# Kernel optimization log

Hardware: AMD Instinct MI355X
Metric: run time of the kernel (lower is better)

## Reference

```python
import jax, jax.numpy as jnp
import numpy as np

N = 100_000
E = 3_200_000
NCLASS = 64
TOPK = 16
NHID = 128
DEGREE = 6


def setup_inputs() -> dict:
    key = jax.random.key(0)
    ks = jax.random.split(key, 8)
    x = jax.random.normal(ks[0], (N, NCLASS), dtype=jnp.float32)
    edge_row = jax.random.randint(ks[1], (E,), 0, N, dtype=jnp.int64)
    edge_col = jax.random.randint(ks[2], (E,), 0, N, dtype=jnp.int64)
    edge_val = jax.random.uniform(ks[3], (E,), dtype=jnp.float32) / 32.0  # ~row-normalized
    # torch.nn.Linear init: U(-1/sqrt(fan_in), 1/sqrt(fan_in))
    lim1 = 1.0 / np.sqrt(TOPK)
    lim2 = 1.0 / np.sqrt(NHID)
    W1 = jax.random.uniform(ks[4], (NHID, TOPK), jnp.float32, -lim1, lim1)
    b1 = jnp.zeros((NHID,), jnp.float32)
    W2 = jax.random.uniform(ks[5], (DEGREE, NHID), jnp.float32, -lim2, lim2)
    b2 = jnp.zeros((DEGREE,), jnp.float32)
    return {"x": x, "edge_row": edge_row, "edge_col": edge_col,
            "edge_val": edge_val, "W1": W1, "b1": b1, "W2": W2, "b2": b2}


def _spmm(edge_row, edge_col, edge_val, h):
    # (adj @ h)[i] = sum_{(i,j) in E} val_ij * h[j]
    return jax.ops.segment_sum(edge_val[:, None] * h[edge_col], edge_row,
                               num_segments=N)


def reference(x, edge_row, edge_col, edge_val, W1, b1, W2, b2):
    # gating: softmax over classes -> top-k probs -> small MLP -> hop weights
    p = jax.nn.softmax(x, axis=1)
    tk, _ = jax.lax.top_k(p, TOPK)                       # [N, TOPK]
    h = jax.nn.leaky_relu(tk @ W1.T + b1, 0.1)           # [N, NHID]
    weight = jax.nn.softmax(h @ W2.T + b2, axis=1)       # [N, DEGREE]
    # dropout is identity in eval mode
    out = weight[:, 0:1] * x
    cur = x
    for i in range(DEGREE - 1):
        cur = _spmm(edge_row, edge_col, edge_val, cur)
        out = out + weight[:, i + 1:i + 2] * cur
    return jax.nn.log_softmax(out, axis=1)
```

## Files before the change

### kernel.cpp

```cpp
#include <hip/hip_runtime.h>
#include <math.h>

#define N_NODES 100000
#define N_EDGES 3200000
#define NCLASS  64
#define TOPK    16
#define NHID    128
#define DEG     6

#define NBUCK   391
#define NSEG    8
#define SEGCAP  1408

#define EB ((N_EDGES + 255) / 256)
#define GNODES 32
#define GB ((N_NODES + GNODES - 1) / GNODES)

__device__ __forceinline__ float bf2f(unsigned short u) {
    return __uint_as_float(((unsigned)u) << 16);
}
__device__ __forceinline__ unsigned short f2bf(float f) {
    unsigned u = __float_as_uint(f);
    u = (u + 0x7FFFu + ((u >> 16) & 1u)) >> 16;
    return (unsigned short)u;
}

__device__ __forceinline__ float wave_max(float v) {
    #pragma unroll
    for (int off = 1; off < 64; off <<= 1) v = fmaxf(v, __shfl_xor(v, off));
    return v;
}
__device__ __forceinline__ float wave_sum(float v) {
    #pragma unroll
    for (int off = 1; off < 64; off <<= 1) v += __shfl_xor(v, off);
    return v;
}

__global__ __launch_bounds__(256) void scatter_gating_kernel(
        const int* __restrict__ erow, const int* __restrict__ ecol,
        const float* __restrict__ eval, int* __restrict__ fill,
        int2* __restrict__ staging,
        const float* __restrict__ x,  const float* __restrict__ W1,
        const float* __restrict__ b1, const float* __restrict__ W2,
        const float* __restrict__ b2, float* __restrict__ weight,
        float* __restrict__ out_acc, unsigned short* __restrict__ xbf) {
    __shared__ float sW1t[TOPK * NHID];
    __shared__ float sb1[NHID];
    __shared__ float sW2[DEG * NHID];
    __shared__ float sb2[DEG];

    if (blockIdx.x < EB) {
        int i = blockIdx.x * 256 + threadIdx.x;
        int s = blockIdx.x & 7;
        if (i < N_EDGES) {
            int   r = __builtin_nontemporal_load(&erow[i]);
            int   c = __builtin_nontemporal_load(&ecol[i]);
            float w = __builtin_nontemporal_load(&eval[i]);
            int b = r >> 8;
            int pos = atomicAdd(&fill[(s * NBUCK + b) * 16], 1);
            if (pos < SEGCAP) {
                int2 e;
                e.x = (c << 8) | (r & 255);
                e.y = __float_as_int(w);
                staging[((size_t)b * NSEG + s) * SEGCAP + pos] = e;
            }
        }
        return;
    }

    int tid = threadIdx.x;
    for (int idx = tid; idx < NHID * TOPK; idx += 256) {
        int k = idx / NHID, j = idx - k * NHID;
        sW1t[idx] = W1[j * TOPK + k];
    }
    for (int i = tid; i < NHID; i += 256) sb1[i] = b1[i];
    for (int i = tid; i < DEG * NHID; i += 256) sW2[i] = W2[i];
    if (tid < DEG) sb2[tid] = b2[tid];
    __syncthreads();

    int wave = tid >> 6;
    int lane = tid & 63;
    int gb = blockIdx.x - EB;

    for (int it = 0; it < GNODES / 4; it++) {
        int node = gb * GNODES + it * 4 + wave;
        if (node >= N_NODES) continue;

        float xv = x[node * NCLASS + lane];
        xbf[node * NCLASS + lane] = f2bf(xv);

        float v = xv;
        #pragma unroll
        for (int k = 2; k <= 64; k <<= 1) {
            #pragma unroll
            for (int j = k >> 1; j > 0; j >>= 1) {
                float o = __shfl_xor(v, j);
                bool keep_small = (((lane & j) == 0) == ((lane & k) == 0));
                v = keep_small ? fminf(v, o) : fmaxf(v, o);
            }
        }
        float m = __shfl(v, 63);
        float e = __expf(v - m);
        float s = wave_sum(e);
        float inv_s = 1.0f / s;

        float h0 = sb1[lane], h1 = sb1[lane + 64];
        #pragma unroll
        for (int k = 0; k < TOPK; k++) {
            float sv = __shfl(v, 63 - k);
            float tk = __expf(sv - m) * inv_s;
            h0 += tk * sW1t[k * NHID + lane];
            h1 += tk * sW1t[k * NHID + lane + 64];
        }
        h0 = (h0 > 0.f) ? h0 : 0.1f * h0;
        h1 = (h1 > 0.f) ? h1 : 0.1f * h1;

        float w[DEG];
        float wm = -1e30f;
        #pragma unroll
        for (int d = 0; d < DEG; d++) {
            float part = h0 * sW2[d * NHID + lane] + h1 * sW2[d * NHID + lane + 64];
            w[d] = wave_sum(part) + sb2[d];
            wm = fmaxf(wm, w[d]);
        }
        float wsum = 0.f;
        #pragma unroll
        for (int d = 0; d < DEG; d++) { w[d] = __expf(w[d] - wm); wsum += w[d]; }
        float inv = 1.0f / wsum;

        if (lane < DEG) weight[node * DEG + lane] = w[lane] * inv;
        out_acc[node * NCLASS + lane] = w[0] * inv * xv;
    }
}

__global__ __launch_bounds__(256) void phase2_build(
        const int2* __restrict__ staging, const int* __restrict__ fill,
        int* __restrict__ row_ptr, int2* __restrict__ edges_s) {
    __shared__ int lred[256];
    __shared__ int lhist[256];
    __shared__ int lscan[256];
    __shared__ int lfill[256];
    __shared__ int sseg[NSEG];
    int b = blockIdx.x, tid = threadIdx.x;

    int part = 0;
    for (int j = tid; j < b; j += 256) {
        int t = 0;
        #pragma unroll
        for (int s = 0; s < NSEG; s++) t += min(fill[(s * NBUCK + j) * 16], SEGCAP);
        part += t;
    }
    lred[tid] = part;
    if (tid < NSEG) sseg[tid] = min(fill[(tid * NBUCK + b) * 16], SEGCAP);
    __syncthreads();
    for (int off = 128; off > 0; off >>= 1) {
        if (tid < off) lred[tid] += lred[tid + off];
        __syncthreads();
    }
    int base_b = lred[0];

    lhist[tid] = 0;
    __syncthreads();
    for (int s = 0; s < NSEG; s++) {
        int c = sseg[s];
        const int2* seg = staging + ((size_t)b * NSEG + s) * SEGCAP;
        for (int j = tid; j < c; j += 256) atomicAdd(&lhist[seg[j].x & 255], 1);
    }
    __syncthreads();
    int v = lhist[tid];
    lscan[tid] = v;
    __syncthreads();
    for (int off = 1; off < 256; off <<= 1) {
        int t = (tid >= off) ? lscan[tid - off] : 0;
        __syncthreads();
        lscan[tid] += t;
        __syncthreads();
    }
    int excl = base_b + (lscan[tid] - v);
    int grow = b * 256 + tid;
    if (grow < N_NODES) row_ptr[grow] = excl;
    if (b == NBUCK - 1 && tid == 255) row_ptr[N_NODES] = excl + v;
    lfill[tid] = excl;
    __syncthreads();
    for (int s = 0; s < NSEG; s++) {
        int c = sseg[s];
        const int2* seg = staging + ((size_t)b * NSEG + s) * SEGCAP;
        for (int j = tid; j < c; j += 256) {
            int2 e = seg[j];
            int rl = e.x & 255;
            int pos = atomicAdd(&lfill[rl], 1);
            edges_s[pos] = make_int2((int)(((unsigned)e.x) >> 8), e.y);
        }
    }
}

__device__ __forceinline__ void gather8(const unsigned short* __restrict__ src,
                                        const long long* __restrict__ edq,
                                        int e, int lane, float& acc) {
    long long q[8];
    #pragma unroll
    for (int k = 0; k < 8; k++) q[k] = __builtin_nontemporal_load(&edq[e + k]);
    float vk[8], fk[8];
    #pragma unroll
    for (int k = 0; k < 8; k++) {
        int col = __builtin_amdgcn_readfirstlane((int)(unsigned)q[k]);
        vk[k] = __int_as_float(__builtin_amdgcn_readfirstlane((int)(q[k] >> 32)));
        fk[k] = bf2f(src[col * NCLASS + lane]);
    }
    #pragma unroll
    for (int k = 0; k < 8; k++) acc += vk[k] * fk[k];
}

__device__ __forceinline__ void gather4(const unsigned short* __restrict__ src,
                                        const long long* __restrict__ edq,
                                        int e, int lane, float& acc) {
    long long q[4];
    #pragma unroll
    for (int k = 0; k < 4; k++) q[k] = __builtin_nontemporal_load(&edq[e + k]);
    float vk[4], fk[4];
    #pragma unroll
    for (int k = 0; k < 4; k++) {
        int col = __builtin_amdgcn_readfirstlane((int)(unsigned)q[k]);
        vk[k] = __int_as_float(__builtin_amdgcn_readfirstlane((int)(q[k] >> 32)));
        fk[k] = bf2f(src[col * NCLASS + lane]);
    }
    #pragma unroll
    for (int k = 0; k < 4; k++) acc += vk[k] * fk[k];
}

__device__ __forceinline__ float drain_row(const unsigned short* __restrict__ src,
                                           const long long* __restrict__ edq,
                                           int e, int end, int lane, float acc) {
    for (; e + 4 <= end; e += 4) gather4(src, edq, e, lane, acc);
    for (; e < end; e++) {
        long long q0 = __builtin_nontemporal_load(&edq[e]);
        int   c0 = __builtin_amdgcn_readfirstlane((int)(unsigned)q0);
        float v0 = __int_as_float(__builtin_amdgcn_readfirstlane((int)(q0 >> 32)));
        acc += v0 * bf2f(src[c0 * NCLASS + lane]);
    }
    return acc;
}

__global__ __launch_bounds__(256) void spmm_kernel(
        const unsigned short* __restrict__ src, unsigned short* __restrict__ dst,
        const unsigned short* __restrict__ prev2,
        const int* __restrict__ row_ptr, const int2* __restrict__ edges_s,
        const float* __restrict__ weight,
        float* __restrict__ out_acc, float* __restrict__ final_out,
        int hop, int mode) {
    int wave = threadIdx.x >> 6;
    int lane = threadIdx.x & 63;
    int wid = blockIdx.x * 4 + wave;
    int rA = wid * 2;
    if (rA >= N_NODES) return;
    int rB = rA + 1;

    int sA   = __builtin_amdgcn_readfirstlane(row_ptr[rA]);
    int endA = __builtin_amdgcn_readfirstlane(row_ptr[rA + 1]);
    int endB = __builtin_amdgcn_readfirstlane(row_ptr[rA + 2]);

    const long long* edq = (const long long*)edges_s;
    float accA = 0.f, accB = 0.f;
    int eA = sA, eB = endA;
    while (eA + 8 <= endA && eB + 8 <= endB) {
        gather8(src, edq, eA, lane, accA);
        gather8(src, edq, eB, lane, accB);
        eA += 8; eB += 8;
    }
    accA = drain_row(src, edq, eA, endA, lane, accA);
    accB = drain_row(src, edq, eB, endB, lane, accB);

    float wA = weight[rA * DEG + hop];
    float wB = weight[rB * DEG + hop];
    if (mode == 0) {
        dst[rA * NCLASS + lane] = f2bf(accA);
        dst[rB * NCLASS + lane] = f2bf(accB);
    } else if (mode == 1) {
        dst[rA * NCLASS + lane] = f2bf(accA);
        dst[rB * NCLASS + lane] = f2bf(accB);
        float pA = bf2f(src[rA * NCLASS + lane]);
        float pB = bf2f(src[rB * NCLASS + lane]);
        float wpA = weight[rA * DEG + hop - 1];
        float wpB = weight[rB * DEG + hop - 1];
        out_acc[rA * NCLASS + lane] += wpA * pA + wA * accA;
        out_acc[rB * NCLASS + lane] += wpB * pB + wB * accB;
    } else {
        float p1A = bf2f(src[rA * NCLASS + lane]);
        float p1B = bf2f(src[rB * NCLASS + lane]);
        float p2A = bf2f(prev2[rA * NCLASS + lane]);
        float p2B = bf2f(prev2[rB * NCLASS + lane]);
        float vA = out_acc[rA * NCLASS + lane]
                 + weight[rA * DEG + hop - 2] * p2A
                 + weight[rA * DEG + hop - 1] * p1A + wA * accA;
        float mA = wave_max(vA);
        float eA2 = __expf(vA - mA);
        float sA2 = wave_sum(eA2);
        final_out[rA * NCLASS + lane] = vA - mA - __logf(sA2);

        float vB = out_acc[rB * NCLASS + lane]
                 + weight[rB * DEG + hop - 2] * p2B
                 + weight[rB * DEG + hop - 1] * p1B + wB * accB;
        float mB = wave_max(vB);
        float eB2 = __expf(vB - mB);
        float sB2 = wave_sum(eB2);
        final_out[rB * NCLASS + lane] = vB - mB - __logf(sB2);
    }
}

extern "C" void kernel_launch(void* const* d_in, const int* in_sizes, int n_in,
                              void* d_out, int out_size, void* d_ws, size_t ws_size,
                              hipStream_t stream) {
    const float* x    = (const float*)d_in[0];
    const int*   erow = (const int*)  d_in[1];
    const int*   ecol = (const int*)  d_in[2];
    const float* eval = (const float*)d_in[3];
    const float* W1   = (const float*)d_in[4];
    const float* b1   = (const float*)d_in[5];
    const float* W2   = (const float*)d_in[6];
    const float* b2   = (const float*)d_in[7];
    float* out = (float*)d_out;

    char* ws = (char*)d_ws;
    size_t off = 0;
    auto alloc = [&](size_t bytes) -> void* {
        void* p = ws + off;
        off = (off + bytes + 255) & ~(size_t)255;
        return p;
    };
    char* regionS = (char*)alloc((size_t)NBUCK * NSEG * SEGCAP * 8);
    int2* staging = (int2*)regionS;
    unsigned short* cur0 = (unsigned short*)regionS;
    unsigned short* cur1 = (unsigned short*)(regionS + (size_t)N_NODES * NCLASS * 2);
    unsigned short* xbf  = (unsigned short*)alloc((size_t)N_NODES * NCLASS * 2);

    int2*  edges_s = (int2*)alloc((size_t)N_EDGES * 8);
    int*   row_ptr = (int*) alloc((size_t)(N_NODES + 1) * 4);
    int*   fill    = (int*) alloc((size_t)NSEG * NBUCK * 16 * 4);
    float* weight  = (float*)alloc((size_t)N_NODES * DEG * 4);

    const int WB = ((N_NODES / 2) + 3) / 4;

    hipMemsetAsync(fill, 0, (size_t)NSEG * NBUCK * 16 * 4, stream);
    scatter_gating_kernel<<<EB + GB, 256, 0, stream>>>(
        erow, ecol, eval, fill, staging, x, W1, b1, W2, b2, weight, out, xbf);
    phase2_build<<<NBUCK, 256, 0, stream>>>(staging, fill, row_ptr, edges_s);

    spmm_kernel<<<WB, 256, 0, stream>>>(xbf,  cur0, cur0, row_ptr, edges_s, weight, out, out, 1, 0);
    spmm_kernel<<<WB, 256, 0, stream>>>(cur0, cur1, cur0, row_ptr, edges_s, weight, out, out, 2, 1);
    spmm_kernel<<<WB, 256, 0, stream>>>(cur1, cur0, cur0, row_ptr, edges_s, weight, out, out, 3, 0);
    spmm_kernel<<<WB, 256, 0, stream>>>(cur0, cur1, cur0, row_ptr, edges_s, weight, out, out, 4, 0);
    spmm_kernel<<<WB, 256, 0, stream>>>(cur1, cur0, cur0, row_ptr, edges_s, weight, out, out, 5, 3);
}
```

Baseline: 682.4 us.

## Interleave gating blocks among scatter blocks and process four rows per wave in SpMM

The fused scatter/gating kernel now interleaves block roles so every fifth block runs gating and the rest scatter edges. Gating work is spread across the grid instead of all running at the tail. The SpMM kernel now has each wave handle four consecutive rows with four independent gather streams instead of two, which exposes more memory-level parallelism per wave. The cost is more registers and half as many waves, which could reduce occupancy or load balance.

Measured after the change: 670.9 us. Within noise of the previous version (-1.7%).

```diff
diff --git a/kernel.cpp b/kernel.cpp
--- a/kernel.cpp
+++ b/kernel.cpp
@@ -49,9 +49,11 @@
     __shared__ float sW2[DEG * NHID];
     __shared__ float sb2[DEG];
 
-    if (blockIdx.x < EB) {
-        int i = blockIdx.x * 256 + threadIdx.x;
-        int s = blockIdx.x & 7;
+    unsigned bi = blockIdx.x;
+    if (bi % 5 != 0) {
+        int sid = (int)(bi - bi / 5u - 1u);
+        int i = sid * 256 + threadIdx.x;
+        int s = sid & 7;
         if (i < N_EDGES) {
             int   r = __builtin_nontemporal_load(&erow[i]);
             int   c = __builtin_nontemporal_load(&ecol[i]);
@@ -68,6 +70,7 @@
         return;
     }
 
+    int gb = (int)(bi / 5u);
     int tid = threadIdx.x;
     for (int idx = tid; idx < NHID * TOPK; idx += 256) {
         int k = idx / NHID, j = idx - k * NHID;
@@ -80,7 +83,6 @@
 
     int wave = tid >> 6;
     int lane = tid & 63;
-    int gb = blockIdx.x - EB;
 
     for (int it = 0; it < GNODES / 4; it++) {
         int node = gb * GNODES + it * 4 + wave;
@@ -251,59 +253,53 @@
     int wave = threadIdx.x >> 6;
     int lane = threadIdx.x & 63;
     int wid = blockIdx.x * 4 + wave;
-    int rA = wid * 2;
-    if (rA >= N_NODES) return;
-    int rB = rA + 1;
-
-    int sA   = __builtin_amdgcn_readfirstlane(row_ptr[rA]);
-    int endA = __builtin_amdgcn_readfirstlane(row_ptr[rA + 1]);
-    int endB = __builtin_amdgcn_readfirstlane(row_ptr[rA + 2]);
+    int r0 = wid * 4;
+    if (r0 >= N_NODES) return;
+
+    int p0 = __builtin_amdgcn_readfirstlane(row_ptr[r0]);
+    int p1 = __builtin_amdgcn_readfirstlane(row_ptr[r0 + 1]);
+    int p2 = __builtin_amdgcn_readfirstlane(row_ptr[r0 + 2]);
+    int p3 = __builtin_amdgcn_readfirstlane(row_ptr[r0 + 3]);
+    int p4 = __builtin_amdgcn_readfirstlane(row_ptr[r0 + 4]);
 
     const long long* edq = (const long long*)edges_s;
-    float accA = 0.f, accB = 0.f;
-    int eA = sA, eB = endA;
-    while (eA + 8 <= endA && eB + 8 <= endB) {
-        gather8(src, edq, eA, lane, accA);
-        gather8(src, edq, eB, lane, accB);
-        eA += 8; eB += 8;
-    }
-    accA = drain_row(src, edq, eA, endA, lane, accA);
-    accB = drain_row(src, edq, eB, endB, lane, accB);
-
-    float wA = weight[rA * DEG + hop];
-    float wB = weight[rB * DEG + hop];
-    if (mode == 0) {
-        dst[rA * NCLASS + lane] = f2bf(accA);
-        dst[rB * NCLASS + lane] = f2bf(accB);
-    } else if (mode == 1) {
-        dst[rA * NCLASS + lane] = f2bf(accA);
-        dst[rB * NCLASS + lane] = f2bf(accB);
-        float pA = bf2f(src[rA * NCLASS + lane]);
-        float pB = bf2f(src[rB * NCLASS + lane]);
-        float wpA = weight[rA * DEG + hop - 1];
-        float wpB = weight[rB * DEG + hop - 1];
-        out_acc[rA * NCLASS + lane] += wpA * pA + wA * accA;
-        out_acc[rB * NCLASS + lane] += wpB * pB + wB * accB;
-    } else {
-        float p1A = bf2f(src[rA * NCLASS + lane]);
-        float p1B = bf2f(src[rB * NCLASS + lane]);
-        float p2A = bf2f(prev2[rA * NCLASS + lane]);
-        float p2B = bf2f(prev2[rB * NCLASS + lane]);
-        float vA = out_acc[rA * NCLASS + lane]
-                 + weight[rA * DEG + hop - 2] * p2A
-                 + weight[rA * DEG + hop - 1] * p1A + wA * accA;
-        float mA = wave_max(vA);
-        float eA2 = __expf(vA - mA);
-        float sA2 = wave_sum(eA2);
-        final_out[rA * NCLASS + lane] = vA - mA - __logf(sA2);
-
-        float vB = out_acc[rB * NCLASS + lane]
-                 + weight[rB * DEG + hop - 2] * p2B
-                 + weight[rB * DEG + hop - 1] * p1B + wB * accB;
-        float mB = wave_max(vB);
-        float eB2 = __expf(vB - mB);
-        float sB2 = wave_sum(eB2);
-        final_out[rB * NCLASS + lane] = vB - mB - __logf(sB2);
+    float acc[4] = {0.f, 0.f, 0.f, 0.f};
+    int e0 = p0, e1 = p1, e2 = p2, e3 = p3;
+    while (e0 + 8 <= p1 && e1 + 8 <= p2 && e2 + 8 <= p3 && e3 + 8 <= p4) {
+        gather8(src, edq, e0, lane, acc[0]);
+        gather8(src, edq, e1, lane, acc[1]);
+        gather8(src, edq, e2, lane, acc[2]);
+        gather8(src, edq, e3, lane, acc[3]);
+        e0 += 8; e1 += 8; e2 += 8; e3 += 8;
+    }
+    acc[0] = drain_row(src, edq, e0, p1, lane, acc[0]);
+    acc[1] = drain_row(src, edq, e1, p2, lane, acc[1]);
+    acc[2] = drain_row(src, edq, e2, p3, lane, acc[2]);
+    acc[3] = drain_row(src, edq, e3, p4, lane, acc[3]);
+
+    #pragma unroll
+    for (int k = 0; k < 4; k++) {
+        int r = r0 + k;
+        float a = acc[k];
+        float w = weight[r * DEG + hop];
+        if (mode == 0) {
+            dst[r * NCLASS + lane] = f2bf(a);
+        } else if (mode == 1) {
+            dst[r * NCLASS + lane] = f2bf(a);
+            float p  = bf2f(src[r * NCLASS + lane]);
+            float wp = weight[r * DEG + hop - 1];
+            out_acc[r * NCLASS + lane] += wp * p + w * a;
+        } else {
+            float q1 = bf2f(src[r * NCLASS + lane]);
+            float q2 = bf2f(prev2[r * NCLASS + lane]);
+            float v = out_acc[r * NCLASS + lane]
+                    + weight[r * DEG + hop - 2] * q2
+                    + weight[r * DEG + hop - 1] * q1 + w * a;
+            float m = wave_max(v);
+            float ee = __expf(v - m);
+            float ss = wave_sum(ee);
+            final_out[r * NCLASS + lane] = v - m - __logf(ss);
+        }
     }
 }
 
@@ -338,7 +334,7 @@
     int*   fill    = (int*) alloc((size_t)NSEG * NBUCK * 16 * 4);
     float* weight  = (float*)alloc((size_t)N_NODES * DEG * 4);
 
-    const int WB = ((N_NODES / 2) + 3) / 4;
+    const int WB = (N_NODES / 4 + 3) / 4;
 
     hipMemsetAsync(fill, 0, (size_t)NSEG * NBUCK * 16 * 4, stream);
     scatter_gating_kernel<<<EB + GB, 256, 0, stream>>>(
```
